# Kernel tuning notes

Measured on AMD Instinct MI355X. Metric: run time of the kernel, lower is better.

Reference implementation:

```python
import jax, jax.numpy as jnp
import numpy as np

T, B, IN, HID, OUT = 100, 2048, 784, 100, 10
BETA = 0.9      # snn.Leaky(beta=0.9)
THRESH = 1.0    # snntorch default threshold
ALPHA = 2.0     # snntorch default ATan surrogate alpha

@jax.custom_vjp
def fire(x):
    # Heaviside spike with ATan surrogate gradient (snntorch default).
    return (x > 0).astype(x.dtype)

def _fire_fwd(x):
    return fire(x), x

def _fire_bwd(x, g):
    return (g * (ALPHA / 2) / (1 + (jnp.pi / 2 * ALPHA * x) ** 2),)

fire.defvjp(_fire_fwd, _fire_bwd)

def setup_inputs() -> dict:
    key = jax.random.key(0)
    k1, k2, k3 = jax.random.split(key, 3)
    x_seq = jax.random.normal(k1, (T, B, IN), dtype=jnp.float32)
    # nn.Linear weights are [out_features, in_features], bias=False
    w1 = jax.random.normal(k2, (HID, IN), dtype=jnp.float32) * (1.0 / np.sqrt(IN))
    w2 = jax.random.normal(k3, (OUT, HID), dtype=jnp.float32) * (1.0 / np.sqrt(HID))
    return {"x_seq": x_seq, "w1": w1, "w2": w2}

def _leaky_step(mem, cur):
    # snntorch Leaky, reset_mechanism='subtract':
    # reset = H(mem_prev - thresh) (detached); mem = beta*mem + input - reset*thresh; spk = fire(mem - thresh)
    reset = jax.lax.stop_gradient((mem > THRESH).astype(mem.dtype))
    mem = BETA * mem + cur - reset * THRESH
    spk = fire(mem - THRESH)
    return spk, mem

def reference(x_seq, w1, w2):
    batch = x_seq.shape[1]
    def step(carry, x_t):
        mem1, mem2 = carry
        spk1, mem1 = _leaky_step(mem1, x_t @ w1.T)      # [B,HID]
        spk2, mem2 = _leaky_step(mem2, spk1 @ w2.T)     # [B,OUT]
        return (mem1, mem2), spk2
    init = (jnp.zeros((batch, HID), x_seq.dtype),
            jnp.zeros((batch, OUT), x_seq.dtype))
    _, spk2_seq = jax.lax.scan(step, init, x_seq)
    return spk2_seq.sum(axis=0)  # spk2_sum: [B, OUT]
```

## Files before the change

kernel.cpp:

```cpp
#include <hip/hip_runtime.h>

#define T_STEPS 100
#define B_SZ    2048
#define IN_DIM  784
#define HID_DIM 100
#define OUT_DIM 10
#define CSTR    100
#define BMR     64
#define KC      16
#define NSTEP   (IN_DIM / KC)
#define XLP     84
#define WLP     112

typedef double f64x4 __attribute__((ext_vector_type(4)));
#define MFMA64(a, b, c) __builtin_amdgcn_mfma_f64_16x16x4f64((a), (b), (c), 0, 0, 0)

__global__ __launch_bounds__(256, 4)
void snn_gemm1(const float* __restrict__ x,
               const float* __restrict__ w1,
               double* __restrict__ cur)
{
  const int tid  = threadIdx.x;
  const int lane = tid & 63;
  const int wv   = tid >> 6;
  const int kg   = lane >> 4;
  const int il   = lane & 15;
  const long rowBase = (long)blockIdx.x * BMR;

  __shared__ float xls[2][KC][XLP];
  __shared__ float wls[2][KC][WLP];

  const int xrow = tid >> 2;
  const int xq   = (tid & 3) * 4;
  const float* xsrc = x + (rowBase + xrow) * (long)IN_DIM + xq;
  const int  wrow = tid >> 1;
  const int  skh  = (tid & 1) * 8;
  const float* wsrc = w1 + (long)wrow * IN_DIM + skh;
  const bool   dow  = tid < 2 * HID_DIM;

  float4 xg, wa, wb;
  auto LOAD = [&](int s) {
    xg = *reinterpret_cast<const float4*>(xsrc + s * KC);
    if (dow) {
      const float4* wp = reinterpret_cast<const float4*>(wsrc + s * KC);
      wa = wp[0]; wb = wp[1];
    }
  };
  auto STORE = [&](int buf) {
    xls[buf][xq + 0][xrow] = xg.x; xls[buf][xq + 1][xrow] = xg.y;
    xls[buf][xq + 2][xrow] = xg.z; xls[buf][xq + 3][xrow] = xg.w;
    if (dow) {
      wls[buf][skh + 0][wrow] = wa.x; wls[buf][skh + 1][wrow] = wa.y;
      wls[buf][skh + 2][wrow] = wa.z; wls[buf][skh + 3][wrow] = wa.w;
      wls[buf][skh + 4][wrow] = wb.x; wls[buf][skh + 5][wrow] = wb.y;
      wls[buf][skh + 6][wrow] = wb.z; wls[buf][skh + 7][wrow] = wb.w;
    }
  };

  LOAD(0);

  f64x4 z = {0.0, 0.0, 0.0, 0.0};
  const double eil = (double)il;
  const double d0 = (kg == 0) ? 1.0 : 0.0;
  const double d1 = (kg == 1) ? 1.0 : 0.0;
  const double d2 = (kg == 2) ? 1.0 : 0.0;
  const double d3 = (kg == 3) ? 1.0 : 0.0;
  const f64x4 Prow0 = MFMA64(eil, d0, z);
  const f64x4 Prow1 = MFMA64(eil, d1, z);
  const f64x4 Pcol0 = MFMA64(d0, eil, z);
  const f64x4 Pcol1 = MFMA64(d1, eil, z);
  const f64x4 Pv0   = MFMA64(d0, d0, z);
  const f64x4 Pv1   = MFMA64(d1, d1, z);
  const f64x4 Pv2   = MFMA64(d2, d2, z);
  const f64x4 Pv3   = MFMA64(d3, d3, z);

  bool okl = true;
  int rowof[4], colof[4];
#pragma unroll
  for (int r = 0; r < 4; ++r) {
    okl = okl && (Pv0[r] == 1.0) && (Pv1[r] == 1.0) && (Pv2[r] == 1.0) && (Pv3[r] == 1.0);
    okl = okl && (Prow0[r] == Prow1[r]) && (Pcol0[r] == Pcol1[r]);
    const int rr = (int)Prow0[r];
    const int cc = (int)Pcol0[r];
    okl = okl && ((double)rr == Prow0[r]) && (rr >= 0) && (rr < 16);
    okl = okl && ((double)cc == Pcol0[r]) && (cc >= 0) && (cc < 16);
    rowof[r] = rr; colof[r] = cc;
  }
  if (__all(okl ? 1 : 0) == 0) {
#pragma unroll
    for (int r = 0; r < 4; ++r) { rowof[r] = kg * 4 + r; colof[r] = il; }
  }

  f64x4 acc[6];
#pragma unroll
  for (int ht = 0; ht < 6; ++ht) acc[ht] = z;
  double acc4[4] = {0.0, 0.0, 0.0, 0.0};

  STORE(0); LOAD(1);
  __syncthreads();

#pragma unroll 1
  for (int s = 0; s < NSTEP; ++s) {
    if (s + 1 < NSTEP) STORE((s + 1) & 1);
    if (s + 2 < NSTEP) LOAD(s + 2);
    const int buf = s & 1;

#pragma unroll
    for (int kk = 0; kk < 4; ++kk) {
      const int kr = kk * 4 + kg;
      const double a0 = (double)xls[buf][kr][wv * 16 + il];
      double b[6];
#pragma unroll
      for (int ht = 0; ht < 6; ++ht)
        b[ht] = (double)wls[buf][kr][ht * 16 + il];
#pragma unroll
      for (int ht = 0; ht < 6; ++ht)
        acc[ht] = MFMA64(a0, b[ht], acc[ht]);
      const float4 wt = *reinterpret_cast<const float4*>(&wls[buf][kr][96]);
      acc4[0] = fma(a0, (double)wt.x, acc4[0]);
      acc4[1] = fma(a0, (double)wt.y, acc4[1]);
      acc4[2] = fma(a0, (double)wt.z, acc4[2]);
      acc4[3] = fma(a0, (double)wt.w, acc4[3]);
    }
    __syncthreads();
  }

#pragma unroll
  for (int c = 0; c < 4; ++c) {
    acc4[c] += __shfl_xor(acc4[c], 16);
    acc4[c] += __shfl_xor(acc4[c], 32);
  }

  const long r0 = rowBase + wv * 16;
#pragma unroll
  for (int ht = 0; ht < 6; ++ht)
#pragma unroll
    for (int m = 0; m < 4; ++m)
      cur[(r0 + rowof[m]) * CSTR + ht * 16 + colof[m]] = acc[ht][m];
  if (kg == 0) {
    double* cp = cur + (r0 + il) * CSTR + 96;
    cp[0] = acc4[0]; cp[1] = acc4[1]; cp[2] = acc4[2]; cp[3] = acc4[3];
  }
}

__global__ __launch_bounds__(256)
void snn_recur(const double* __restrict__ cur,
               const float* __restrict__ w2,
               double* __restrict__ mem1s, float* __restrict__ spk1s,
               double* __restrict__ mem2s, float* __restrict__ spk2s,
               float* __restrict__ outs,
               float* __restrict__ dout,
               int chunkT, int isFirst, int isLast)
{
  const int tid = threadIdx.x;
  const int b0  = blockIdx.x * 4;
  __shared__ float w2l[OUT_DIM * HID_DIM];
  __shared__ float spkl[2][4 * HID_DIM];

  if (tid < 250)
    reinterpret_cast<float4*>(w2l)[tid] = reinterpret_cast<const float4*>(w2)[tid];

  const bool pa = tid < 100;
  const int  sl = tid / 25, q4 = (tid % 25) * 4;
  const long aOff = (long)(b0 + sl) * HID_DIM + q4;
  double m1[4] = {0.0, 0.0, 0.0, 0.0};
  float4 s1 = make_float4(0.f, 0.f, 0.f, 0.f);
  if (pa && !isFirst) {
    const double2* mp = reinterpret_cast<const double2*>(mem1s + aOff);
    double2 a = mp[0], b = mp[1];
    m1[0] = a.x; m1[1] = a.y; m1[2] = b.x; m1[3] = b.y;
    s1 = *reinterpret_cast<const float4*>(spk1s + aOff);
  }

  const bool pb = tid < 80;
  const int  pp = tid >> 1, hf = tid & 1;
  const int  ss = pp / 10, oo = pp % 10;
  const long bOff = (long)b0 * OUT_DIM + pp;
  double m2 = 0.0;
  float s2 = 0.f, oacc = 0.f;
  if (pb && !isFirst && hf == 0) { m2 = mem2s[bOff]; s2 = spk2s[bOff]; oacc = outs[bOff]; }

  __syncthreads();

  double2 ca0, cb0, ca1, cb1;
  if (pa) {
    const double2* cp0 = reinterpret_cast<const double2*>(cur + aOff);
    ca0 = cp0[0]; cb0 = cp0[1];
    const int t1 = (chunkT > 1) ? 1 : 0;
    const double2* cp1 = reinterpret_cast<const double2*>(
        cur + (long)t1 * B_SZ * HID_DIM + aOff);
    ca1 = cp1[0]; cb1 = cp1[1];
  }

  for (int tt = 0; tt < chunkT; tt += 2) {
    const bool two = (tt + 1 < chunkT);
    if (pa) {
      double cu0[4] = {ca0.x, ca0.y, cb0.x, cb0.y};
      double cu1[4] = {ca1.x, ca1.y, cb1.x, cb1.y};
      const int tn2 = (tt + 2 < chunkT) ? tt + 2 : chunkT - 1;
      const int tn3 = (tt + 3 < chunkT) ? tt + 3 : chunkT - 1;
      const double2* cp2 = reinterpret_cast<const double2*>(
          cur + (long)tn2 * B_SZ * HID_DIM + aOff);
      ca0 = cp2[0]; cb0 = cp2[1];
      const double2* cp3 = reinterpret_cast<const double2*>(
          cur + (long)tn3 * B_SZ * HID_DIM + aOff);
      ca1 = cp3[0]; cb1 = cp3[1];

      float4 sp0, sp1;
      float* sp0v = &sp0.x; float* sp1v = &sp1.x;
      const float* s1v = &s1.x;
#pragma unroll
      for (int j = 0; j < 4; ++j) {
        double m = 0.9 * m1[j];
        m = m + cu0[j];
        m = m - (double)s1v[j];
        sp0v[j] = (m > 1.0) ? 1.0f : 0.0f;
        m1[j] = m;
      }
      if (two) {
#pragma unroll
        for (int j = 0; j < 4; ++j) {
          double m = 0.9 * m1[j];
          m = m + cu1[j];
          m = m - (double)sp0v[j];
          sp1v[j] = (m > 1.0) ? 1.0f : 0.0f;
          m1[j] = m;
        }
        s1 = sp1;
      } else {
        s1 = sp0;
      }
      *reinterpret_cast<float4*>(&spkl[0][sl * HID_DIM + q4]) = sp0;
      if (two)
        *reinterpret_cast<float4*>(&spkl[1][sl * HID_DIM + q4]) = sp1;
    }
    __syncthreads();
    if (pb) {
      const float* wr = &w2l[oo * HID_DIM] + hf * 50;
#pragma unroll 1
      for (int u = 0; u < 2; ++u) {
        if (u == 1 && !two) break;
        const float* sr = &spkl[u][ss * HID_DIM] + hf * 50;
        double a0 = 0.0, a1 = 0.0;
#pragma unroll
        for (int h = 0; h < 50; h += 2) {
          a0 = fma((double)sr[h],     (double)wr[h],     a0);
          a1 = fma((double)sr[h + 1], (double)wr[h + 1], a1);
        }
        double a = a0 + a1;
        a = a + __shfl_xor(a, 1);
        if (hf == 0) {
          double m = 0.9 * m2;
          m = m + a;
          m = m - (double)s2;
          const float sp = (m > 1.0) ? 1.0f : 0.0f;
          m2 = m; s2 = sp; oacc += sp;
        }
      }
    }
    __syncthreads();
  }

  if (pa) {
    double2* mp = reinterpret_cast<double2*>(mem1s + aOff);
    mp[0] = make_double2(m1[0], m1[1]);
    mp[1] = make_double2(m1[2], m1[3]);
    *reinterpret_cast<float4*>(spk1s + aOff) = s1;
  }
  if (pb && hf == 0) {
    mem2s[bOff] = m2; spk2s[bOff] = s2; outs[bOff] = oacc;
    if (isLast) dout[bOff] = oacc;
  }
}

extern "C" void kernel_launch(void* const* d_in, const int* in_sizes, int n_in,
                              void* d_out, int out_size, void* d_ws, size_t ws_size,
                              hipStream_t stream) {
  const float* x  = (const float*)d_in[0];
  const float* w1 = (const float*)d_in[1];
  const float* w2 = (const float*)d_in[2];
  float* out = (float*)d_out;

  char* ws = (char*)d_ws;
  double* mem1s = (double*)(ws);
  float*  spk1s = (float*) (ws + 1638400);
  double* mem2s = (double*)(ws + 2457600);
  float*  spk2s = (float*) (ws + 2621440);
  float*  outs  = (float*) (ws + 2703360);
  double* cur   = (double*)(ws + 2785280);

  const size_t perT = (size_t)B_SZ * HID_DIM * 8;
  size_t curCap = ws_size > (size_t)2785280 ? ws_size - 2785280 : 0;
  int Tc = (int)(curCap / perT);
  if (Tc > T_STEPS) Tc = T_STEPS;
  if (Tc < 1) Tc = 1;

  for (int t0 = 0; t0 < T_STEPS; t0 += Tc) {
    const int ct = (T_STEPS - t0 < Tc) ? (T_STEPS - t0) : Tc;
    snn_gemm1<<<dim3(ct * (B_SZ / BMR)), dim3(256), 0, stream>>>(
        x + (size_t)t0 * B_SZ * IN_DIM, w1, cur);
    snn_recur<<<dim3(B_SZ / 4), dim3(256), 0, stream>>>(
        cur, w2, mem1s, spk1s, mem2s, spk2s, outs, out,
        ct, (t0 == 0) ? 1 : 0, (t0 + ct >= T_STEPS) ? 1 : 0);
  }
}
```

Baseline: 675.8 us.

## Load x directly into registers and stage padded w1 in large LDS chunks

The GEMM1 kernel stops staging x through shared memory. Each lane now reads its own 8 consecutive x values from global memory into registers, prefetching one step ahead. w1 is first padded to K=800 by a new small kernel, and the GEMM then stages it in 160-wide K chunks in LDS with fewer barriers. The aim is to cut LDS traffic, transposing stores and synchronisation per K-step, at the cost of a larger LDS footprint (launch bounds lowered to 2 blocks per CU), an extra kernel launch, and less coalesced per-lane x reads.

```diff
diff --git a/kernel.cpp b/kernel.cpp
--- a/kernel.cpp
+++ b/kernel.cpp
@@ -3,21 +3,30 @@
 #define T_STEPS 100
 #define B_SZ    2048
 #define IN_DIM  784
+#define KPAD    800
 #define HID_DIM 100
 #define OUT_DIM 10
 #define CSTR    100
 #define BMR     64
-#define KC      16
-#define NSTEP   (IN_DIM / KC)
-#define XLP     84
-#define WLP     112
+#define CHUNK   160
+#define NCHUNK  5
+#define SPC     5
+#define KSTEPS  25
+#define WROW    102
 
 typedef double f64x4 __attribute__((ext_vector_type(4)));
 #define MFMA64(a, b, c) __builtin_amdgcn_mfma_f64_16x16x4f64((a), (b), (c), 0, 0, 0)
 
-__global__ __launch_bounds__(256, 4)
+__global__ void pad_w1(const float* __restrict__ w1, float* __restrict__ w1p) {
+  int i = blockIdx.x * 256 + threadIdx.x;
+  if (i >= HID_DIM * KPAD) return;
+  int r = i / KPAD, k = i % KPAD;
+  w1p[i] = (k < IN_DIM) ? w1[r * IN_DIM + k] : 0.0f;
+}
+
+__global__ __launch_bounds__(256, 2)
 void snn_gemm1(const float* __restrict__ x,
-               const float* __restrict__ w1,
+               const float* __restrict__ w1p,
                double* __restrict__ cur)
 {
   const int tid  = threadIdx.x;
@@ -25,39 +34,25 @@
   const int wv   = tid >> 6;
   const int kg   = lane >> 4;
   const int il   = lane & 15;
+  const int kg8  = kg * 8;
   const long rowBase = (long)blockIdx.x * BMR;
 
-  __shared__ float xls[2][KC][XLP];
-  __shared__ float wls[2][KC][WLP];
-
-  const int xrow = tid >> 2;
-  const int xq   = (tid & 3) * 4;
-  const float* xsrc = x + (rowBase + xrow) * (long)IN_DIM + xq;
-  const int  wrow = tid >> 1;
-  const int  skh  = (tid & 1) * 8;
-  const float* wsrc = w1 + (long)wrow * IN_DIM + skh;
-  const bool   dow  = tid < 2 * HID_DIM;
-
-  float4 xg, wa, wb;
-  auto LOAD = [&](int s) {
-    xg = *reinterpret_cast<const float4*>(xsrc + s * KC);
-    if (dow) {
-      const float4* wp = reinterpret_cast<const float4*>(wsrc + s * KC);
-      wa = wp[0]; wb = wp[1];
+  __shared__ float wls[CHUNK][WROW];
+
+  const float* xrp = x + (rowBase + wv * 16 + il) * (long)IN_DIM;
+  float xcur[8], xnxt[8];
+  auto XLOAD = [&](int S, float* d) {
+    if (S == KSTEPS - 1 && kg >= 2) {
+#pragma unroll
+      for (int j = 0; j < 8; ++j) d[j] = 0.0f;
+    } else {
+      const float* p = xrp + S * 32 + kg8;
+      *reinterpret_cast<float4*>(&d[0]) = *reinterpret_cast<const float4*>(p);
+      *reinterpret_cast<float4*>(&d[4]) = *reinterpret_cast<const float4*>(p + 4);
     }
   };
-  auto STORE = [&](int buf) {
-    xls[buf][xq + 0][xrow] = xg.x; xls[buf][xq + 1][xrow] = xg.y;
-    xls[buf][xq + 2][xrow] = xg.z; xls[buf][xq + 3][xrow] = xg.w;
-    if (dow) {
-      wls[buf][skh + 0][wrow] = wa.x; wls[buf][skh + 1][wrow] = wa.y;
-      wls[buf][skh + 2][wrow] = wa.z; wls[buf][skh + 3][wrow] = wa.w;
-      wls[buf][skh + 4][wrow] = wb.x; wls[buf][skh + 5][wrow] = wb.y;
-      wls[buf][skh + 6][wrow] = wb.z; wls[buf][skh + 7][wrow] = wb.w;
-    }
-  };
-
-  LOAD(0);
+
+  XLOAD(0, xcur);
 
   f64x4 z = {0.0, 0.0, 0.0, 0.0};
   const double eil = (double)il;
@@ -96,39 +91,56 @@
   for (int ht = 0; ht < 6; ++ht) acc[ht] = z;
   double acc4[4] = {0.0, 0.0, 0.0, 0.0};
 
-  STORE(0); LOAD(1);
-  __syncthreads();
-
 #pragma unroll 1
-  for (int s = 0; s < NSTEP; ++s) {
-    if (s + 1 < NSTEP) STORE((s + 1) & 1);
-    if (s + 2 < NSTEP) LOAD(s + 2);
-    const int buf = s & 1;
-
-#pragma unroll
-    for (int kk = 0; kk < 4; ++kk) {
-      const int kr = kk * 4 + kg;
-      const double a0 = (double)xls[buf][kr][wv * 16 + il];
-      double b[6];
-#pragma unroll
-      for (int ht = 0; ht < 6; ++ht)
-        b[ht] = (double)wls[buf][kr][ht * 16 + il];
-#pragma unroll
-      for (int ht = 0; ht < 6; ++ht)
-        acc[ht] = MFMA64(a0, b[ht], acc[ht]);
-      const float4 wt = *reinterpret_cast<const float4*>(&wls[buf][kr][96]);
-      acc4[0] = fma(a0, (double)wt.x, acc4[0]);
-      acc4[1] = fma(a0, (double)wt.y, acc4[1]);
-      acc4[2] = fma(a0, (double)wt.z, acc4[2]);
-      acc4[3] = fma(a0, (double)wt.w, acc4[3]);
+  for (int c = 0; c < NCHUNK; ++c) {
+#pragma unroll 1
+    for (int i = 0; i < 16; ++i) {
+      const int idx = i * 256 + tid;
+      if (idx < HID_DIM * (CHUNK / 4)) {
+        const int r  = idx / (CHUNK / 4);
+        const int kq = idx % (CHUNK / 4);
+        const float4 wg = *reinterpret_cast<const float4*>(
+            w1p + (long)r * KPAD + c * CHUNK + kq * 4);
+        wls[kq * 4 + 0][r] = wg.x;
+        wls[kq * 4 + 1][r] = wg.y;
+        wls[kq * 4 + 2][r] = wg.z;
+        wls[kq * 4 + 3][r] = wg.w;
+      }
     }
     __syncthreads();
-  }
-
-#pragma unroll
-  for (int c = 0; c < 4; ++c) {
-    acc4[c] += __shfl_xor(acc4[c], 16);
-    acc4[c] += __shfl_xor(acc4[c], 32);
+
+#pragma unroll 1
+    for (int ls = 0; ls < SPC; ++ls) {
+      const int S = c * SPC + ls;
+      if (S + 1 < KSTEPS) XLOAD(S + 1, xnxt);
+      const int kb = ls * 32 + kg8;
+
+#pragma unroll
+      for (int m = 0; m < 8; ++m) {
+        const double a0 = (double)xcur[m];
+        double b[6];
+#pragma unroll
+        for (int ht = 0; ht < 6; ++ht)
+          b[ht] = (double)wls[kb + m][ht * 16 + il];
+#pragma unroll
+        for (int ht = 0; ht < 6; ++ht)
+          acc[ht] = MFMA64(a0, b[ht], acc[ht]);
+        const float4 wt = *reinterpret_cast<const float4*>(&wls[kb + m][96]);
+        acc4[0] = fma(a0, (double)wt.x, acc4[0]);
+        acc4[1] = fma(a0, (double)wt.y, acc4[1]);
+        acc4[2] = fma(a0, (double)wt.z, acc4[2]);
+        acc4[3] = fma(a0, (double)wt.w, acc4[3]);
+      }
+#pragma unroll
+      for (int j = 0; j < 8; ++j) xcur[j] = xnxt[j];
+    }
+    __syncthreads();
+  }
+
+#pragma unroll
+  for (int cc2 = 0; cc2 < 4; ++cc2) {
+    acc4[cc2] += __shfl_xor(acc4[cc2], 16);
+    acc4[cc2] += __shfl_xor(acc4[cc2], 32);
   }
 
   const long r0 = rowBase + wv * 16;
@@ -282,15 +294,18 @@
   float* out = (float*)d_out;
 
   char* ws = (char*)d_ws;
-  double* mem1s = (double*)(ws);
-  float*  spk1s = (float*) (ws + 1638400);
-  double* mem2s = (double*)(ws + 2457600);
-  float*  spk2s = (float*) (ws + 2621440);
-  float*  outs  = (float*) (ws + 2703360);
-  double* cur   = (double*)(ws + 2785280);
+  float*  w1p   = (float*) (ws);
+  double* mem1s = (double*)(ws +  320000);
+  float*  spk1s = (float*) (ws + 1958400);
+  double* mem2s = (double*)(ws + 2777600);
+  float*  spk2s = (float*) (ws + 2941440);
+  float*  outs  = (float*) (ws + 3023360);
+  double* cur   = (double*)(ws + 3105280);
+
+  pad_w1<<<dim3((HID_DIM * KPAD + 255) / 256), dim3(256), 0, stream>>>(w1, w1p);
 
   const size_t perT = (size_t)B_SZ * HID_DIM * 8;
-  size_t curCap = ws_size > (size_t)2785280 ? ws_size - 2785280 : 0;
+  size_t curCap = ws_size > (size_t)3105280 ? ws_size - 3105280 : 0;
   int Tc = (int)(curCap / perT);
   if (Tc > T_STEPS) Tc = T_STEPS;
   if (Tc < 1) Tc = 1;
@@ -298,7 +313,7 @@
   for (int t0 = 0; t0 < T_STEPS; t0 += Tc) {
     const int ct = (T_STEPS - t0 < Tc) ? (T_STEPS - t0) : Tc;
     snn_gemm1<<<dim3(ct * (B_SZ / BMR)), dim3(256), 0, stream>>>(
-        x + (size_t)t0 * B_SZ * IN_DIM, w1, cur);
+        x + (size_t)t0 * B_SZ * IN_DIM, w1p, cur);
     snn_recur<<<dim3(B_SZ / 4), dim3(256), 0, stream>>>(
         cur, w2, mem1s, spk1s, mem2s, spk2s, outs, out,
         ct, (t0 == 0) ? 1 : 0, (t0 + ct >= T_STEPS) ? 1 : 0);
```

New measurement: 877.2 us. 29.8% more time.
